# Performance work log

Measured on AMD Instinct MI355X. Metric: run time of the kernel, lower is better.

The kernel has to match this reference:

```python
import jax, jax.numpy as jnp
import numpy as np

DROPOUT_RATE = 0.25
STRIDE = 5  # must be odd


def setup_inputs() -> dict:
    key = jax.random.key(0)
    k1, k2 = jax.random.split(key)
    b, c, h, w = 4, 256, 64, 64
    x = jax.random.normal(k1, (b, c, h, w), dtype=jnp.float32)
    # uniform randoms underlying the dropout mask on the expanded grid
    rand_vals = jax.random.uniform(k2, (h * STRIDE, w * STRIDE), dtype=jnp.float32)
    return {"x": x, "rand_vals": rand_vals}


def reference(x, rand_vals):
    s = STRIDE
    s2 = s // 2
    rate = DROPOUT_RATE
    b, c, h, w = x.shape
    # zero-pad spatial dims by s//2 (ZeroPad2d)
    xp = jnp.pad(x, ((0, 0), (0, 0), (s2, s2), (s2, s2)))
    # x_new[:, :, i*s+p, j*s+q] = xp[:, :, i+p, j+q]  -> single fused gather
    idx_h = (jnp.arange(h)[:, None] + jnp.arange(s)[None, :]).reshape(h * s)  # [h*s]
    idx_w = (jnp.arange(w)[:, None] + jnp.arange(s)[None, :]).reshape(w * s)  # [w*s]
    x_new = xp[:, :, idx_h[:, None], idx_w[None, :]]  # [b, c, h*s, w*s]
    # dropout mask with forced keep at each patch center (s2 + i*s, s2 + j*s)
    mask = rand_vals > rate
    mask = mask.at[s2::s, s2::s].set(True)
    return x_new * mask.astype(x_new.dtype) / (1.0 - rate)
```

## Files before the change

### kernel.cpp

```cpp
#include <hip/hip_runtime.h>
#include <stdint.h>


#define KEEP_SCALE (1.0f / 0.75f)

typedef float f32x4 __attribute__((ext_vector_type(4)));

__global__ __launch_bounds__(256) void build_mask_kernel(
    const float* __restrict__ rv,
    uint32_t* __restrict__ mask)
{
    const int g  = blockIdx.x * 256 + threadIdx.x;
    const int oh = g / 320;
    const int ow = g - oh * 320;

    int qh = oh / 5, rh = oh - qh * 5;
    int ih = qh + rh - 2;
    int q  = ow / 5, r  = ow - q * 5;
    int iw = q + r - 2;

    float v = rv[g];
    bool keep = ((v > 0.25f) || (rh == 2 && r == 2))
                && ((unsigned)ih < 64u) && ((unsigned)iw < 64u);

    unsigned long long bal = __ballot(keep);
    int lane = threadIdx.x & 63;
    if (lane == 0)
        mask[g >> 5] = (uint32_t)bal;
    else if (lane == 32)
        mask[g >> 5] = (uint32_t)(bal >> 32);
}

__global__ __launch_bounds__(512) void expand_cps_dropout_kernel(
    const float* __restrict__ x,
    const uint32_t* __restrict__ mask,
    float* __restrict__ out)
{
    __shared__ __align__(16) float    xs[12 * 64];
    __shared__ __align__(16) uint32_t ms[320];

    const int t  = threadIdx.x;
    const int b  = blockIdx.x;
    const int bc = b / 10;
    const int rg = b - bc * 10;

    const int a = 32 * rg;
    int s0 = a / 5 - 2;
    s0 = s0 < 0 ? 0 : (s0 > 52 ? 52 : s0);

    if (t < 192) {
        const float* xsrc = x + (size_t)bc * 4096 + s0 * 64;
        __builtin_amdgcn_global_load_lds(
            (const __attribute__((address_space(1))) void*)(xsrc + t * 4),
            (__attribute__((address_space(3))) void*)(xs + (t & ~63) * 4),
            16, 0, 0);
    } else if (t < 272) {
        int i = t - 192;
        const uint32_t* msrc = mask + rg * 320;
        __builtin_amdgcn_global_load_lds(
            (const __attribute__((address_space(1))) void*)(msrc + i * 4),
            (__attribute__((address_space(3))) void*)(ms + (i & ~63) * 4),
            16, 0, 0);
    }

    int      xoffB[5][4];
    int      rowB[5];
    int      soffF[5];
    int      midx[5];
    uint32_t msh_[5];
    #pragma unroll
    for (int ji = 0; ji < 5; ++ji) {
        int f  = t + 512 * ji;
        int r0 = f / 80;
        int o4 = f - r0 * 80;
        int ow = o4 * 4;
        soffF[ji] = r0 * 320 + ow;
        msh_[ji]  = (uint32_t)((o4 & 7) * 4);
        midx[ji]  = r0 * 10 + (o4 >> 3);
        int oh = a + r0;
        int q = oh / 5, r = oh - q * 5;
        int ihrel = q + r - 2 - s0;
        ihrel = ihrel < 0 ? 0 : (ihrel > 11 ? 11 : ihrel);
        rowB[ji] = ihrel * 256;
        #pragma unroll
        for (int k = 0; k < 4; ++k) {
            int o = ow + k;
            int qq = o / 5, rr = o - qq * 5;
            int iw = qq + rr - 2;
            iw = iw < 0 ? 0 : (iw > 63 ? 63 : iw);
            xoffB[ji][k] = iw * 4;
        }
    }

    __syncthreads();

    uint32_t mb[5];
    #pragma unroll
    for (int ji = 0; ji < 5; ++ji)
        mb[ji] = ms[midx[ji]] >> msh_[ji];

    float* ob = out + (size_t)b * 10240;
    const char* xsb = (const char*)xs;

    #pragma unroll
    for (int ji = 0; ji < 5; ++ji) {
        const char* xr = xsb + rowB[ji];
        uint32_t m = mb[ji];
        f32x4 o;
        o.x = (m & 1u) ? *(const float*)(xr + xoffB[ji][0]) * KEEP_SCALE : 0.0f;
        o.y = (m & 2u) ? *(const float*)(xr + xoffB[ji][1]) * KEEP_SCALE : 0.0f;
        o.z = (m & 4u) ? *(const float*)(xr + xoffB[ji][2]) * KEEP_SCALE : 0.0f;
        o.w = (m & 8u) ? *(const float*)(xr + xoffB[ji][3]) * KEEP_SCALE : 0.0f;
        *reinterpret_cast<f32x4*>(ob + soffF[ji]) = o;
    }
}

extern "C" void kernel_launch(void* const* d_in, const int* in_sizes, int n_in,
                              void* d_out, int out_size, void* d_ws, size_t ws_size,
                              hipStream_t stream) {
    const float* x  = (const float*)d_in[0];
    const float* rv = (const float*)d_in[1];
    float* out      = (float*)d_out;
    uint32_t* mask  = (uint32_t*)d_ws;

    hipLaunchKernelGGL(build_mask_kernel, dim3(400), dim3(256), 0, stream, rv, mask);

    dim3 block(512);
    dim3 grid(10240);
    hipLaunchKernelGGL(expand_cps_dropout_kernel, grid, block, 0, stream,
                       x, mask, out);
}
```

Baseline: 83.02 us.

## Drop LDS staging and gather input directly from global memory

Removes the shared-memory staging of input rows and mask words (async global-to-LDS loads plus a block barrier). Each thread now reads the mask word and input elements straight from global memory, relying on L1/L2 caching. Blocks shrink to 256 threads covering 16 output rows, which doubles the grid. This avoids barrier and LDS latency but adds redundant uncached-path global loads and per-element index math.

```diff
diff --git a/kernel.cpp b/kernel.cpp
--- a/kernel.cpp
+++ b/kernel.cpp
@@ -31,87 +31,48 @@
         mask[g >> 5] = (uint32_t)(bal >> 32);
 }
 
-__global__ __launch_bounds__(512) void expand_cps_dropout_kernel(
+__global__ __launch_bounds__(256) void expand_cps_dropout_kernel(
     const float* __restrict__ x,
     const uint32_t* __restrict__ mask,
     float* __restrict__ out)
 {
-    __shared__ __align__(16) float    xs[12 * 64];
-    __shared__ __align__(16) uint32_t ms[320];
-
     const int t  = threadIdx.x;
     const int b  = blockIdx.x;
-    const int bc = b / 10;
-    const int rg = b - bc * 10;
+    const int bc = b / 20;
+    const int rg = b - bc * 20;
+    const int a  = 16 * rg;
 
-    const int a = 32 * rg;
-    int s0 = a / 5 - 2;
-    s0 = s0 < 0 ? 0 : (s0 > 52 ? 52 : s0);
-
-    if (t < 192) {
-        const float* xsrc = x + (size_t)bc * 4096 + s0 * 64;
-        __builtin_amdgcn_global_load_lds(
-            (const __attribute__((address_space(1))) void*)(xsrc + t * 4),
-            (__attribute__((address_space(3))) void*)(xs + (t & ~63) * 4),
-            16, 0, 0);
-    } else if (t < 272) {
-        int i = t - 192;
-        const uint32_t* msrc = mask + rg * 320;
-        __builtin_amdgcn_global_load_lds(
-            (const __attribute__((address_space(1))) void*)(msrc + i * 4),
-            (__attribute__((address_space(3))) void*)(ms + (i & ~63) * 4),
-            16, 0, 0);
-    }
-
-    int      xoffB[5][4];
-    int      rowB[5];
-    int      soffF[5];
-    int      midx[5];
-    uint32_t msh_[5];
-    #pragma unroll
-    for (int ji = 0; ji < 5; ++ji) {
-        int f  = t + 512 * ji;
-        int r0 = f / 80;
-        int o4 = f - r0 * 80;
-        int ow = o4 * 4;
-        soffF[ji] = r0 * 320 + ow;
-        msh_[ji]  = (uint32_t)((o4 & 7) * 4);
-        midx[ji]  = r0 * 10 + (o4 >> 3);
-        int oh = a + r0;
-        int q = oh / 5, r = oh - q * 5;
-        int ihrel = q + r - 2 - s0;
-        ihrel = ihrel < 0 ? 0 : (ihrel > 11 ? 11 : ihrel);
-        rowB[ji] = ihrel * 256;
-        #pragma unroll
-        for (int k = 0; k < 4; ++k) {
-            int o = ow + k;
-            int qq = o / 5, rr = o - qq * 5;
-            int iw = qq + rr - 2;
-            iw = iw < 0 ? 0 : (iw > 63 ? 63 : iw);
-            xoffB[ji][k] = iw * 4;
-        }
-    }
-
-    __syncthreads();
-
-    uint32_t mb[5];
-    #pragma unroll
-    for (int ji = 0; ji < 5; ++ji)
-        mb[ji] = ms[midx[ji]] >> msh_[ji];
-
-    float* ob = out + (size_t)b * 10240;
-    const char* xsb = (const char*)xs;
+    const float*    xim  = x + (size_t)bc * 4096;
+    const uint32_t* mrow = mask + rg * 160;
+    float*          ob   = out + (size_t)b * 5120;
 
     #pragma unroll
     for (int ji = 0; ji < 5; ++ji) {
-        const char* xr = xsb + rowB[ji];
-        uint32_t m = mb[ji];
+        const int f  = t + 256 * ji;
+        const int r0 = f / 80;
+        const int o4 = f - r0 * 80;
+        const int ow = o4 * 4;
+
+        const int oh = a + r0;
+        const int qh = oh / 5;
+        const int rh = oh - qh * 5;
+        int ih = qh + rh - 2;
+        ih = ih < 0 ? 0 : (ih > 63 ? 63 : ih);
+        const float* xr = xim + ih * 64;
+
+        const uint32_t mb = mrow[r0 * 10 + (o4 >> 3)] >> ((o4 & 7) * 4);
+
         f32x4 o;
-        o.x = (m & 1u) ? *(const float*)(xr + xoffB[ji][0]) * KEEP_SCALE : 0.0f;
-        o.y = (m & 2u) ? *(const float*)(xr + xoffB[ji][1]) * KEEP_SCALE : 0.0f;
-        o.z = (m & 4u) ? *(const float*)(xr + xoffB[ji][2]) * KEEP_SCALE : 0.0f;
-        o.w = (m & 8u) ? *(const float*)(xr + xoffB[ji][3]) * KEEP_SCALE : 0.0f;
-        *reinterpret_cast<f32x4*>(ob + soffF[ji]) = o;
+        #pragma unroll
+        for (int k = 0; k < 4; ++k) {
+            int oo = ow + k;
+            int q  = oo / 5;
+            int r  = oo - q * 5;
+            int iw = q + r - 2;
+            iw = iw < 0 ? 0 : (iw > 63 ? 63 : iw);
+            o[k] = (mb & (1u << k)) ? xr[iw] * KEEP_SCALE : 0.0f;
+        }
+        *reinterpret_cast<f32x4*>(ob + 4 * f) = o;
     }
 }
 
@@ -125,8 +86,8 @@
 
     hipLaunchKernelGGL(build_mask_kernel, dim3(400), dim3(256), 0, stream, rv, mask);
 
-    dim3 block(512);
-    dim3 grid(10240);
+    dim3 block(256);
+    dim3 grid(20480);
     hipLaunchKernelGGL(expand_cps_dropout_kernel, grid, block, 0, stream,
                        x, mask, out);
 }
```

Result: slower. 148.3 us (+78.6%).
